# Kernel tuning notes

Measured on AMD Instinct MI355X. Metric: run time of the kernel, lower is better.

Reference implementation:

```python
import jax, jax.numpy as jnp
import numpy as np

IGNORE_INDEX = -100
BETA = 0.1
ALPHA = 1.0  # HFAlignmentLoss default; nll term is zero since compute_nll_loss=False

B, T, H, V = 4, 512, 2048, 32000


def setup_inputs() -> dict:
    key = jax.random.key(0)
    k1, k2, k3, k4, k5 = jax.random.split(key, 5)
    scale = 1.0 / np.sqrt(H)
    return {
        "x": jax.random.normal(k1, (B, T, H), dtype=jnp.float32),
        "ref_x": jax.random.normal(k2, (B, T, H), dtype=jnp.float32),
        "y": jax.random.randint(k3, (B, T), 0, V, dtype=jnp.int64),
        "W": jax.random.normal(k4, (V, H), dtype=jnp.float32) * scale,
        "ref_W": jax.random.normal(k5, (V, H), dtype=jnp.float32) * scale,
    }


def _batch_logps(logits, labels):
    """Average per-token label log-prob over non-ignored tokens (average_log_prob=True).
    logits: (B, T, V) float32; labels: (B, T) int. Returns (B,) float32."""
    mask = labels != IGNORE_INDEX
    safe_labels = jnp.where(mask, labels, 0)
    logps = jax.nn.log_softmax(logits, axis=-1)                       # (B, T, V)
    per_tok = jnp.take_along_axis(logps, safe_labels[..., None], axis=-1)[..., 0]
    maskf = mask.astype(logits.dtype)
    return (per_tok * maskf).sum(-1) / maskf.sum(-1)                  # (B,)


def reference(x, ref_x, y, W, ref_W):
    half = x.shape[0] // 2

    # policy LM head (bias=False) -> logits in fp32 (HF ref casts with .float())
    logits = jnp.einsum("bth,vh->btv", x, W).astype(jnp.float32)
    all_logps = _batch_logps(logits, y)
    policy_chosen_logps = all_logps[:half]
    policy_rejected_logps = all_logps[half:]

    # reference LM head (ref_bias=False)
    ref_logits = jnp.einsum("bth,vh->btv", ref_x, ref_W).astype(jnp.float32)
    ref_all_logps = _batch_logps(ref_logits, y)
    ref_chosen_logps = ref_all_logps[:half]
    ref_rejected_logps = ref_all_logps[half:]

    # SPPO-hard alignment loss
    a = policy_chosen_logps - ref_chosen_logps
    b = policy_rejected_logps - ref_rejected_logps
    chosen_rewards = BETA * a
    rejected_rewards = BETA * b
    losses = (a - 0.5 / BETA) ** 2 + (b + 0.5 / BETA) ** 2

    policy_nll_loss = jnp.float32(0.0)  # compute_nll_loss=False
    loss = policy_nll_loss * ALPHA - losses.mean()
    return loss


if __name__ == "__main__":
    out = reference(**setup_inputs())
    print(out)
```

## Files before the change

### kernel.cpp

```cpp
#include <hip/hip_runtime.h>
#include <hip/hip_bf16.h>
#include <math.h>

#define H 2048
#define V 32000
#define T 512
#define TOK 2048
#define IGN (-100)

#define BM 64
#define BN 64
#define BK 32
#define NCH (V / BN)

#define GBM 128
#define GBN 128
#define GBK 32

typedef unsigned short u16;
typedef __attribute__((ext_vector_type(8))) short short8;
typedef __attribute__((ext_vector_type(4))) float f32x4;

__device__ __forceinline__ u16 f2bf(float f) {
    unsigned int u = __float_as_uint(f);
    u += 0x7fffu + ((u >> 16) & 1u);
    return (u16)(u >> 16);
}

#define GLD16(gp, lp) __builtin_amdgcn_global_load_lds( \
    (const __attribute__((address_space(1))) unsigned int*)(gp), \
    (__attribute__((address_space(3))) unsigned int*)(lp), 16, 0, 0)

__global__ __launch_bounds__(256) void f32_to_bf16(
    const float* __restrict__ src, u16* __restrict__ dst, int n4)
{
    for (int i = blockIdx.x * 256 + threadIdx.x; i < n4; i += gridDim.x * 256) {
        float4 v = ((const float4*)src)[i];
        ushort4 o;
        o.x = f2bf(v.x); o.y = f2bf(v.y); o.z = f2bf(v.z); o.w = f2bf(v.w);
        ((ushort4*)dst)[i] = o;
    }
}

__global__ __launch_bounds__(256) void gemm_bf16(
    const u16* __restrict__ Xb, const u16* __restrict__ Wb,
    float* __restrict__ ms_m, float* __restrict__ ms_s)
{
    __shared__ __align__(16) u16 lds[2 * GBM * GBK];

    const int tid  = threadIdx.x;
    const int wave = tid >> 6;
    const int lane = tid & 63;
    const int q    = lane >> 4;
    const int rl   = lane & 15;
    const int m0   = (wave >> 1) * 64;
    const int n0   = (wave & 1) * 64;
    const int model = blockIdx.z;
    const size_t tokBase = (size_t)blockIdx.x * GBM;
    const size_t vBase   = (size_t)blockIdx.y * GBN;

    const u16* __restrict__ A  = Xb + (size_t)model * (2048ULL * H) + tokBase * H;
    const u16* __restrict__ Bm = Wb + (size_t)model * ((size_t)V * H) + vBase * H;

    const int G0 = wave * 128 + lane;
    const int G1 = G0 + 64;
    const int r0 = G0 >> 2, g0 = (((G0 & 3) ^ ((r0 >> 1) & 3)) << 3);
    const int r1 = G1 >> 2, g1 = (((G1 & 3) ^ ((r1 >> 1) & 3)) << 3);
    const u16* a0 = A  + (size_t)r0 * H + g0;
    const u16* a1 = A  + (size_t)r1 * H + g1;
    const u16* b0 = Bm + (size_t)r0 * H + g0;
    const u16* b1 = Bm + (size_t)r1 * H + g1;
    u16* lA0 = lds + wave * 1024;
    u16* lA1 = lA0 + 512;
    u16* lB0 = lds + 4096 + wave * 1024;
    u16* lB1 = lB0 + 512;

    int aOff[4], bOff[4];
#pragma unroll
    for (int im = 0; im < 4; im++) {
        int r = m0 + im * 16 + rl;
        aOff[im] = r * 32 + ((q ^ ((r >> 1) & 3)) << 3);
    }
#pragma unroll
    for (int in = 0; in < 4; in++) {
        int r = n0 + in * 16 + rl;
        bOff[in] = 4096 + r * 32 + ((q ^ ((r >> 1) & 3)) << 3);
    }

    f32x4 acc[4][4];
#pragma unroll
    for (int a = 0; a < 4; a++)
#pragma unroll
        for (int b = 0; b < 4; b++)
            acc[a][b] = (f32x4){0.f, 0.f, 0.f, 0.f};

    for (int k0 = 0; k0 < H; k0 += GBK) {
        __syncthreads();
        GLD16(a0 + k0, lA0);
        GLD16(a1 + k0, lA1);
        GLD16(b0 + k0, lB0);
        GLD16(b1 + k0, lB1);
        __syncthreads();

        short8 aF[4], bF[4];
#pragma unroll
        for (int im = 0; im < 4; im++) aF[im] = *(const short8*)&lds[aOff[im]];
#pragma unroll
        for (int in = 0; in < 4; in++) bF[in] = *(const short8*)&lds[bOff[in]];

#pragma unroll
        for (int im = 0; im < 4; im++)
#pragma unroll
            for (int in = 0; in < 4; in++)
                acc[im][in] = __builtin_amdgcn_mfma_f32_16x16x32_bf16(
                    aF[im], bF[in], acc[im][in], 0, 0, 0);
    }

    const int chunk = (int)blockIdx.y * 2 + (n0 >> 6);
#pragma unroll
    for (int im = 0; im < 4; im++) {
#pragma unroll
        for (int i = 0; i < 4; i++) {
            float mx = fmaxf(fmaxf(acc[im][0][i], acc[im][1][i]),
                             fmaxf(acc[im][2][i], acc[im][3][i]));
#pragma unroll
            for (int off = 1; off < 16; off <<= 1)
                mx = fmaxf(mx, __shfl_xor(mx, off));
            float s = __expf(acc[im][0][i] - mx) + __expf(acc[im][1][i] - mx)
                    + __expf(acc[im][2][i] - mx) + __expf(acc[im][3][i] - mx);
#pragma unroll
            for (int off = 1; off < 16; off <<= 1)
                s += __shfl_xor(s, off);
            if (rl == 0) {
                int row = m0 + im * 16 + q * 4 + i;
                size_t idx = ((size_t)model * TOK + tokBase + row) * NCH + chunk;
                ms_m[idx] = mx;
                ms_s[idx] = s;
            }
        }
    }
}

__global__ __launch_bounds__(256) void gemm_partial(
    const float* __restrict__ X,  const float* __restrict__ Xr,
    const float* __restrict__ Wp, const float* __restrict__ Wr,
    float* __restrict__ ms_m, float* __restrict__ ms_s)
{
    __shared__ float smemF[64 * 65];
    short* smemS = (short*)smemF;
    short* ldsA = smemS;
    short* ldsB = smemS + 64 * 40;

    const int tid     = threadIdx.x;
    const int model   = blockIdx.z;
    const int tokBase = blockIdx.x * BM;
    const int vBase   = blockIdx.y * BN;

    const float* __restrict__ Xp = model ? Xr : X;
    const float* __restrict__ Wm = model ? Wr : Wp;

    const int lane = tid & 63;
    const int wave = tid >> 6;
    const int q    = lane >> 4;
    const int rl   = lane & 15;
    const int m0   = (wave >> 1) * 32;
    const int n0   = (wave & 1) * 32;

    f32x4 acc[2][2];
    for (int a = 0; a < 2; a++)
        for (int b = 0; b < 2; b++)
            acc[a][b] = (f32x4){0.f, 0.f, 0.f, 0.f};

    for (int kk = 0; kk < H / BK; kk++) {
        const int k0 = kk * BK;
        __syncthreads();
        for (int rep = 0; rep < 2; rep++) {
            int i   = tid + rep * 256;
            int row = i >> 3;
            int cf  = (i & 7) * 4;
            const float4 va = *(const float4*)(Xp + (size_t)(tokBase + row) * H + k0 + cf);
            short* pa = ldsA + row * 40 + cf;
            pa[0] = (short)f2bf(va.x); pa[1] = (short)f2bf(va.y);
            pa[2] = (short)f2bf(va.z); pa[3] = (short)f2bf(va.w);
            const float4 vb = *(const float4*)(Wm + (size_t)(vBase + row) * H + k0 + cf);
            short* pb = ldsB + row * 40 + cf;
            pb[0] = (short)f2bf(vb.x); pb[1] = (short)f2bf(vb.y);
            pb[2] = (short)f2bf(vb.z); pb[3] = (short)f2bf(vb.w);
        }
        __syncthreads();

        short8 aF[2], bF[2];
        for (int im = 0; im < 2; im++)
            aF[im] = *(const short8*)(ldsA + (m0 + im * 16 + rl) * 40 + q * 8);
        for (int in = 0; in < 2; in++)
            bF[in] = *(const short8*)(ldsB + (n0 + in * 16 + rl) * 40 + q * 8);

        for (int im = 0; im < 2; im++)
            for (int in = 0; in < 2; in++)
                acc[im][in] = __builtin_amdgcn_mfma_f32_16x16x32_bf16(
                    aF[im], bF[in], acc[im][in], 0, 0, 0);
    }

    __syncthreads();
    for (int im = 0; im < 2; im++)
        for (int in = 0; in < 2; in++)
            for (int i = 0; i < 4; i++)
                smemF[(m0 + im * 16 + q * 4 + i) * 65 + (n0 + in * 16 + rl)] =
                    acc[im][in][i];
    __syncthreads();

    if (tid < 64) {
        const float* rowp = smemF + tid * 65;
        float m = -INFINITY;
        for (int j = 0; j < 64; j++) m = fmaxf(m, rowp[j]);
        float s = 0.f;
        for (int j = 0; j < 64; j++) s += __expf(rowp[j] - m);
        size_t idx = ((size_t)model * TOK + (tokBase + tid)) * NCH + blockIdx.y;
        ms_m[idx] = m;
        ms_s[idx] = s;
    }
}

__global__ __launch_bounds__(256) void label_logit(
    const float* __restrict__ X,  const float* __restrict__ Xr,
    const float* __restrict__ Wp, const float* __restrict__ Wr,
    const int* __restrict__ y, float* __restrict__ z)
{
    int id    = blockIdx.x * 4 + (threadIdx.x >> 6);
    int lane  = threadIdx.x & 63;
    int model = id >> 11;
    int token = id & 2047;
    const float* __restrict__ Xp = model ? Xr : X;
    const float* __restrict__ Wm = model ? Wr : Wp;
    int lab = y[token];
    float sum = 0.f;
    if (lab != IGN) {
        const float* xp = Xp + (size_t)token * H;
        const float* wp = Wm + (size_t)lab * H;
        for (int c = lane; c < H; c += 64) sum += xp[c] * wp[c];
    }
    for (int off = 32; off; off >>= 1) sum += __shfl_down(sum, off);
    if (lane == 0) z[id] = sum;
}

__global__ __launch_bounds__(256) void lse_logp(
    const float* __restrict__ ms_m, const float* __restrict__ ms_s,
    const float* __restrict__ z, float* __restrict__ logp)
{
    int id = blockIdx.x;
    int t  = threadIdx.x;
    __shared__ float red[256];
    const float* mrow = ms_m + (size_t)id * NCH;
    const float* srow = ms_s + (size_t)id * NCH;

    float m = -INFINITY;
    for (int c = t; c < NCH; c += 256) m = fmaxf(m, mrow[c]);
    red[t] = m; __syncthreads();
    for (int w = 128; w; w >>= 1) {
        if (t < w) red[t] = fmaxf(red[t], red[t + w]);
        __syncthreads();
    }
    float M = red[0]; __syncthreads();

    float s = 0.f;
    for (int c = t; c < NCH; c += 256) s += srow[c] * __expf(mrow[c] - M);
    red[t] = s; __syncthreads();
    for (int w = 128; w; w >>= 1) {
        if (t < w) red[t] += red[t + w];
        __syncthreads();
    }
    if (t == 0) {
        float lse = M + logf(red[0]);
        logp[id] = z[id] - lse;
    }
}

__global__ void final_loss(const float* __restrict__ logp,
                           const int* __restrict__ y,
                           float* __restrict__ out)
{
    __shared__ float lp[8];
    int t = threadIdx.x;
    if (t < 8) {
        int model = t >> 2, b = t & 3;
        float s = 0.f, cnt = 0.f;
        for (int i = 0; i < T; i++) {
            int tok = b * T + i;
            if (y[tok] != IGN) { s += logp[model * TOK + tok]; cnt += 1.f; }
        }
        lp[t] = s / cnt;
    }
    __syncthreads();
    if (t == 0) {
        float a0 = lp[0] - lp[4], a1 = lp[1] - lp[5];
        float b0 = lp[2] - lp[6], b1 = lp[3] - lp[7];
        float l0 = (a0 - 5.f) * (a0 - 5.f) + (b0 + 5.f) * (b0 + 5.f);
        float l1 = (a1 - 5.f) * (a1 - 5.f) + (b1 + 5.f) * (b1 + 5.f);
        out[0] = -(l0 + l1) * 0.5f;
    }
}

extern "C" void kernel_launch(void* const* d_in, const int* in_sizes, int n_in,
                              void* d_out, int out_size, void* d_ws, size_t ws_size,
                              hipStream_t stream)
{
    const float* X  = (const float*)d_in[0];
    const float* Xr = (const float*)d_in[1];
    const int*   y  = (const int*)d_in[2];
    const float* Wp = (const float*)d_in[3];
    const float* Wr = (const float*)d_in[4];
    float* out = (float*)d_out;

    float* ws   = (float*)d_ws;
    const size_t msElems = (size_t)2 * TOK * NCH;
    float* ms_m = ws;
    float* ms_s = ws + msElems;
    float* z    = ws + 2 * msElems;
    float* logp = z + 2 * TOK;
    u16*   Xb   = (u16*)(logp + 2 * TOK);
    u16*   Wb   = Xb + (size_t)2 * 2048 * H;

    const size_t NEED = 2 * msElems * 4 + 4 * 2 * TOK * 4
                      + (size_t)2 * 2048 * H * 2 + (size_t)2 * V * H * 2;

    if (ws_size >= NEED) {
        f32_to_bf16<<<1024, 256, 0, stream>>>(X,  Xb,                 (2048 * H) / 4);
        f32_to_bf16<<<1024, 256, 0, stream>>>(Xr, Xb + 2048 * H,      (2048 * H) / 4);
        f32_to_bf16<<<4096, 256, 0, stream>>>(Wp, Wb,                 (V * H) / 4);
        f32_to_bf16<<<4096, 256, 0, stream>>>(Wr, Wb + (size_t)V * H, (V * H) / 4);

        dim3 gg(TOK / GBM, V / GBN, 2);
        gemm_bf16<<<gg, 256, 0, stream>>>(Xb, Wb, ms_m, ms_s);
    } else {
        dim3 g1(TOK / BM, V / BN, 2);
        gemm_partial<<<g1, 256, 0, stream>>>(X, Xr, Wp, Wr, ms_m, ms_s);
    }

    label_logit<<<(2 * TOK) / 4, 256, 0, stream>>>(X, Xr, Wp, Wr, y, z);
    lse_logp<<<2 * TOK, 256, 0, stream>>>(ms_m, ms_s, z, logp);
    final_loss<<<1, 64, 0, stream>>>(logp, y, out);
}
```

Baseline: 1.299 ms.

## Rewrite bf16 GEMM as 256x256 tile with 8 waves and pipelined LDS prefetch

Replaces the 128x128 single-buffered bf16 GEMM with a 256x256-tile, 512-thread kernel. It double-buffers 64-wide K slices in 128KB of LDS and interleaves global-to-LDS staging with MFMA quadrants, using explicit barriers, waitcnt and setprio. Blocks are remapped over a 1D grid so neighbouring workgroups share tiles for better L2 reuse. The larger tiles cut LDS and global traffic per FLOP, at the cost of high register pressure and fragile hand-tuned vmcnt synchronisation.

```diff
diff --git a/kernel.cpp b/kernel.cpp
--- a/kernel.cpp
+++ b/kernel.cpp
@@ -13,10 +13,6 @@
 #define BK 32
 #define NCH (V / BN)
 
-#define GBM 128
-#define GBN 128
-#define GBK 32
-
 typedef unsigned short u16;
 typedef __attribute__((ext_vector_type(8))) short short8;
 typedef __attribute__((ext_vector_type(4))) float f32x4;
@@ -42,103 +38,182 @@
     }
 }
 
-__global__ __launch_bounds__(256) void gemm_bf16(
+__global__ __launch_bounds__(512, 2) void gemm_bf16(
     const u16* __restrict__ Xb, const u16* __restrict__ Wb,
     float* __restrict__ ms_m, float* __restrict__ ms_s)
 {
-    __shared__ __align__(16) u16 lds[2 * GBM * GBK];
+    __shared__ __align__(16) u16 lds[65536];
 
     const int tid  = threadIdx.x;
     const int wave = tid >> 6;
     const int lane = tid & 63;
     const int q    = lane >> 4;
     const int rl   = lane & 15;
-    const int m0   = (wave >> 1) * 64;
-    const int n0   = (wave & 1) * 64;
-    const int model = blockIdx.z;
-    const size_t tokBase = (size_t)blockIdx.x * GBM;
-    const size_t vBase   = (size_t)blockIdx.y * GBN;
+    const int wm   = wave >> 2;
+    const int wn   = wave & 3;
+
+    const int lin = (int)blockIdx.x;
+    const int wg  = (lin & 7) * 250 + (lin >> 3);
+    const int bx  = wg & 7;
+    const int rem = wg >> 3;
+    const int by  = rem % 125;
+    const int model = rem / 125;
+
+    const size_t tokBase = (size_t)bx * 256;
+    const size_t vBase   = (size_t)by * 256;
 
     const u16* __restrict__ A  = Xb + (size_t)model * (2048ULL * H) + tokBase * H;
     const u16* __restrict__ Bm = Wb + (size_t)model * ((size_t)V * H) + vBase * H;
-
-    const int G0 = wave * 128 + lane;
-    const int G1 = G0 + 64;
-    const int r0 = G0 >> 2, g0 = (((G0 & 3) ^ ((r0 >> 1) & 3)) << 3);
-    const int r1 = G1 >> 2, g1 = (((G1 & 3) ^ ((r1 >> 1) & 3)) << 3);
-    const u16* a0 = A  + (size_t)r0 * H + g0;
-    const u16* a1 = A  + (size_t)r1 * H + g1;
-    const u16* b0 = Bm + (size_t)r0 * H + g0;
-    const u16* b1 = Bm + (size_t)r1 * H + g1;
-    u16* lA0 = lds + wave * 1024;
-    u16* lA1 = lA0 + 512;
-    u16* lB0 = lds + 4096 + wave * 1024;
-    u16* lB1 = lB0 + 512;
-
-    int aOff[4], bOff[4];
-#pragma unroll
-    for (int im = 0; im < 4; im++) {
-        int r = m0 + im * 16 + rl;
-        aOff[im] = r * 32 + ((q ^ ((r >> 1) & 3)) << 3);
-    }
-#pragma unroll
-    for (int in = 0; in < 4; in++) {
-        int r = n0 + in * 16 + rl;
-        bOff[in] = 4096 + r * 32 + ((q ^ ((r >> 1) & 3)) << 3);
-    }
-
-    f32x4 acc[4][4];
-#pragma unroll
-    for (int a = 0; a < 4; a++)
-#pragma unroll
-        for (int b = 0; b < 4; b++)
-            acc[a][b] = (f32x4){0.f, 0.f, 0.f, 0.f};
-
-    for (int k0 = 0; k0 < H; k0 += GBK) {
-        __syncthreads();
-        GLD16(a0 + k0, lA0);
-        GLD16(a1 + k0, lA1);
-        GLD16(b0 + k0, lB0);
-        GLD16(b1 + k0, lB1);
-        __syncthreads();
-
-        short8 aF[4], bF[4];
-#pragma unroll
-        for (int im = 0; im < 4; im++) aF[im] = *(const short8*)&lds[aOff[im]];
-#pragma unroll
-        for (int in = 0; in < 4; in++) bF[in] = *(const short8*)&lds[bOff[in]];
-
-#pragma unroll
-        for (int im = 0; im < 4; im++)
-#pragma unroll
-            for (int in = 0; in < 4; in++)
-                acc[im][in] = __builtin_amdgcn_mfma_f32_16x16x32_bf16(
-                    aF[im], bF[in], acc[im][in], 0, 0, 0);
-    }
-
-    const int chunk = (int)blockIdx.y * 2 + (n0 >> 6);
-#pragma unroll
-    for (int im = 0; im < 4; im++) {
-#pragma unroll
-        for (int i = 0; i < 4; i++) {
-            float mx = fmaxf(fmaxf(acc[im][0][i], acc[im][1][i]),
-                             fmaxf(acc[im][2][i], acc[im][3][i]));
+    const u16* __restrict__ A1p = A  + 128 * H;
+    const u16* __restrict__ B1p = Bm + 128 * H;
+
+    const int G0 = wave * 64 + lane;
+    const int G1 = G0 + 512;
+    const int r0 = G0 >> 3, s0 = (G0 & 7) ^ (r0 & 7);
+    const int r1 = G1 >> 3, s1 = (G1 & 7) ^ (r1 & 7);
+    const int off0 = r0 * H + s0 * 8;
+    const int off1 = r1 * H + s1 * 8;
+    const int ldsS0 = wave * 512;
+    const int ldsS1 = 4096 + wave * 512;
+
+#define STAGE(gp, hb) do { \
+    GLD16((gp) + off0, lds + (hb) + ldsS0); \
+    GLD16((gp) + off1, lds + (hb) + ldsS1); \
+} while (0)
+
+    const int sB = (q ^ (rl & 7)) << 3;
+    int aoff[8], boff[4];
+#pragma unroll
+    for (int im = 0; im < 8; ++im) aoff[im] = (im * 16 + rl) * 64 + sB;
+#pragma unroll
+    for (int in = 0; in < 4; ++in) boff[in] = ((wn & 1) * 64 + in * 16 + rl) * 64 + sB;
+
+    const int aB0 = wm * 8192;
+    const int aB1 = 32768 + wm * 8192;
+    const int bB0 = 16384 + (wn >> 1) * 8192;
+    const int bB1 = 49152 + (wn >> 1) * 8192;
+
+    short8 af[4][2], bf[4][2];
+    f32x4 acc[8][4];
+#pragma unroll
+    for (int a = 0; a < 8; ++a)
+#pragma unroll
+        for (int b = 0; b < 4; ++b) acc[a][b] = (f32x4){0.f, 0.f, 0.f, 0.f};
+
+#define LDA(cb, mh) do { \
+    _Pragma("unroll") \
+    for (int f = 0; f < 4; ++f) { \
+        const int o_ = (cb) + aoff[(mh) * 4 + f]; \
+        af[f][0] = *(const short8*)(lds + o_); \
+        af[f][1] = *(const short8*)(lds + (o_ ^ 32)); \
+    } } while (0)
+
+#define LDB(cb) do { \
+    _Pragma("unroll") \
+    for (int f = 0; f < 4; ++f) { \
+        const int o_ = (cb) + boff[f]; \
+        bf[f][0] = *(const short8*)(lds + o_); \
+        bf[f][1] = *(const short8*)(lds + (o_ ^ 32)); \
+    } } while (0)
+
+#define QUAD(mh, nh) do { \
+    _Pragma("unroll") \
+    for (int f = 0; f < 4; ++f) \
+    _Pragma("unroll") \
+    for (int g = 0; g < 2; ++g) { \
+        acc[(mh)*4+f][(nh)*2+g] = __builtin_amdgcn_mfma_f32_16x16x32_bf16( \
+            af[f][0], bf[(nh)*2+g][0], acc[(mh)*4+f][(nh)*2+g], 0, 0, 0); \
+        acc[(mh)*4+f][(nh)*2+g] = __builtin_amdgcn_mfma_f32_16x16x32_bf16( \
+            af[f][1], bf[(nh)*2+g][1], acc[(mh)*4+f][(nh)*2+g], 0, 0, 0); \
+    } } while (0)
+
+#define SYNC_PRE() do { \
+    __builtin_amdgcn_s_barrier(); \
+    asm volatile("s_waitcnt lgkmcnt(0)" ::: "memory"); \
+    __builtin_amdgcn_s_setprio(1); \
+} while (0)
+
+#define SYNC_POST() do { \
+    __builtin_amdgcn_s_setprio(0); \
+    __builtin_amdgcn_s_barrier(); \
+    asm volatile("" ::: "memory"); \
+} while (0)
+
+    STAGE(Bm,        16384); STAGE(B1p,       24576);
+    STAGE(A,             0); STAGE(A1p,        8192);
+    STAGE(Bm + 64,   49152); STAGE(B1p + 64,  57344);
+    STAGE(A + 64,    32768);
+    asm volatile("s_waitcnt vmcnt(6)" ::: "memory");
+    __builtin_amdgcn_s_barrier();
+    asm volatile("" ::: "memory");
+
+#pragma unroll 1
+    for (int i = 0; i < 15; ++i) {
+        const int k1 = i * 128 + 64, k2 = k1 + 64, k3 = k2 + 64;
+        LDA(aB0, 0); LDB(bB0);
+        STAGE(A1p + k1, 40960);
+        SYNC_PRE(); QUAD(0, 0); SYNC_POST();
+        STAGE(Bm + k2, 16384);
+        SYNC_PRE(); QUAD(0, 1); SYNC_POST();
+        LDA(aB0, 1);
+        STAGE(B1p + k2, 24576);
+        SYNC_PRE(); QUAD(1, 1); SYNC_POST();
+        STAGE(A + k2, 0);
+        asm volatile("s_waitcnt vmcnt(6)" ::: "memory");
+        SYNC_PRE(); QUAD(1, 0); SYNC_POST();
+        LDA(aB1, 0); LDB(bB1);
+        STAGE(A1p + k2, 8192);
+        SYNC_PRE(); QUAD(0, 0); SYNC_POST();
+        STAGE(Bm + k3, 49152);
+        SYNC_PRE(); QUAD(0, 1); SYNC_POST();
+        LDA(aB1, 1);
+        STAGE(B1p + k3, 57344);
+        SYNC_PRE(); QUAD(1, 1); SYNC_POST();
+        STAGE(A + k3, 32768);
+        asm volatile("s_waitcnt vmcnt(6)" ::: "memory");
+        SYNC_PRE(); QUAD(1, 0); SYNC_POST();
+    }
+
+    STAGE(A1p + 31 * 64, 40960);
+    asm volatile("s_waitcnt vmcnt(0)" ::: "memory");
+    __builtin_amdgcn_s_barrier();
+    asm volatile("" ::: "memory");
+
+    LDA(aB0, 0); LDB(bB0); QUAD(0, 0); QUAD(0, 1);
+    LDA(aB0, 1);           QUAD(1, 0); QUAD(1, 1);
+    LDA(aB1, 0); LDB(bB1); QUAD(0, 0); QUAD(0, 1);
+    LDA(aB1, 1);           QUAD(1, 0); QUAD(1, 1);
+
+    const int chunk = by * 4 + wn;
+    const size_t rowB = (size_t)model * TOK + tokBase + (size_t)wm * 128;
+#pragma unroll
+    for (int im = 0; im < 8; ++im) {
+#pragma unroll
+        for (int i2 = 0; i2 < 4; ++i2) {
+            float v0 = acc[im][0][i2], v1 = acc[im][1][i2];
+            float v2 = acc[im][2][i2], v3 = acc[im][3][i2];
+            float mx = fmaxf(fmaxf(v0, v1), fmaxf(v2, v3));
 #pragma unroll
             for (int off = 1; off < 16; off <<= 1)
                 mx = fmaxf(mx, __shfl_xor(mx, off));
-            float s = __expf(acc[im][0][i] - mx) + __expf(acc[im][1][i] - mx)
-                    + __expf(acc[im][2][i] - mx) + __expf(acc[im][3][i] - mx);
+            float s = __expf(v0 - mx) + __expf(v1 - mx)
+                    + __expf(v2 - mx) + __expf(v3 - mx);
 #pragma unroll
             for (int off = 1; off < 16; off <<= 1)
                 s += __shfl_xor(s, off);
             if (rl == 0) {
-                int row = m0 + im * 16 + q * 4 + i;
-                size_t idx = ((size_t)model * TOK + tokBase + row) * NCH + chunk;
+                size_t idx = (rowB + im * 16 + q * 4 + i2) * NCH + chunk;
                 ms_m[idx] = mx;
                 ms_s[idx] = s;
             }
         }
     }
+#undef STAGE
+#undef LDA
+#undef LDB
+#undef QUAD
+#undef SYNC_PRE
+#undef SYNC_POST
 }
 
 __global__ __launch_bounds__(256) void gemm_partial(
@@ -329,8 +404,8 @@
         f32_to_bf16<<<4096, 256, 0, stream>>>(Wp, Wb,                 (V * H) / 4);
         f32_to_bf16<<<4096, 256, 0, stream>>>(Wr, Wb + (size_t)V * H, (V * H) / 4);
 
-        dim3 gg(TOK / GBM, V / GBN, 2);
-        gemm_bf16<<<gg, 256, 0, stream>>>(Xb, Wb, ms_m, ms_s);
+        dim3 gg(2000);
+        gemm_bf16<<<gg, 512, 0, stream>>>(Xb, Wb, ms_m, ms_s);
     } else {
         dim3 g1(TOK / BM, V / BN, 2);
         gemm_partial<<<g1, 256, 0, stream>>>(X, Xr, Wp, Wr, ms_m, ms_s);
```

New measurement: 1.142 ms. 1.14x faster.
